# Optimization experiments

Measured on AMD Instinct MI355X. Metric: run time of the kernel, lower is better.

Reference implementation:

```python
import jax, jax.numpy as jnp
import numpy as np

N_LEAVES = 32768
DEPTH = 16               # tree levels, leaves at level 0
N_NODES = 2 * N_LEAVES - 1
H = 256                  # h_size
X = 300                  # x_size
FEAT = 1024              # image feature_size
R = 49                   # image regions
VOCAB = 30000
CLASSES = 5


def setup_inputs() -> dict:
    ks = jax.random.split(jax.random.key(0), 10)
    wordid = jax.random.randint(ks[0], (N_NODES,), 0, VOCAB, dtype=jnp.int32)
    # leaves carry word tokens (mask=1), internal nodes don't (mask=0)
    mask = jnp.concatenate([jnp.ones(N_LEAVES, jnp.int32),
                            jnp.zeros(N_NODES - N_LEAVES, jnp.int32)])
    image = jax.random.normal(ks[1], (R, FEAT), dtype=jnp.float32)
    h0 = jnp.zeros((N_NODES, H), jnp.float32)
    c0 = jnp.zeros((N_NODES, H), jnp.float32)
    s = lambda k, shp, fan: jax.random.normal(k, shp, dtype=jnp.float32) * (1.0 / np.sqrt(fan))
    emb = s(ks[2], (VOCAB, X), X)
    attn_w_in = s(ks[3], (X, FEAT), FEAT)            # Attention.linear_in (no bias)
    attn_w_out = s(ks[4], (X, X + FEAT), X + FEAT)   # Attention.linear_out
    attn_b_out = jnp.zeros((X,), jnp.float32)
    w_iou = s(ks[5], (3 * H, X), X)                  # cell.W_iou (no bias)
    u_iou = s(ks[6], (3 * H, 2 * H), 2 * H)          # cell.U_iou (no bias)
    b_iou = jnp.zeros((1, 3 * H), jnp.float32)
    u_f_w = s(ks[7], (2 * H, 2 * H), 2 * H)          # cell.U_f
    u_f_b = jnp.zeros((2 * H,), jnp.float32)
    lin_w = s(ks[8], (CLASSES, H), H)                # final classifier
    lin_b = jnp.zeros((CLASSES,), jnp.float32)
    return dict(wordid=wordid, mask=mask, image=image, h0=h0, c0=c0, emb=emb,
                attn_w_in=attn_w_in, attn_w_out=attn_w_out, attn_b_out=attn_b_out,
                w_iou=w_iou, u_iou=u_iou, b_iou=b_iou, u_f_w=u_f_w, u_f_b=u_f_b,
                lin_w=lin_w, lin_b=lin_b)


def _forward(wordid, mask, image, h0, c0, emb, attn_w_in, attn_w_out, attn_b_out,
             w_iou, u_iou, b_iou, u_f_w, u_f_b, lin_w, lin_b):
    # --- embedding + attention over image regions ---
    embeds = emb[wordid * mask]                                  # [N, X]
    img_in = image @ attn_w_in.T                                 # [R, X]
    atten = jax.nn.softmax(embeds @ img_in.T, axis=1)            # [N, R]
    context = atten @ image                                      # [N, FEAT]
    sent = jnp.tanh(jnp.concatenate([context, embeds], axis=1) @ attn_w_out.T + attn_b_out)
    iou_x = (sent @ w_iou.T) * mask[:, None].astype(sent.dtype)  # [N, 3H] (dropout p=0 -> identity)

    def apply_node(iou, c_in):
        i, o, u = jnp.split(iou + b_iou, 3, axis=1)
        c_new = jax.nn.sigmoid(i) * jnp.tanh(u) + c_in
        return jax.nn.sigmoid(o) * jnp.tanh(c_new), c_new

    # --- leaves: no mailbox, apply_node with initial c ---
    h_leaf, c_leaf = apply_node(iou_x[:N_LEAVES], c0[:N_LEAVES])
    h = h0.at[:N_LEAVES].set(h_leaf)
    c = c0.at[:N_LEAVES].set(c_leaf)

    # --- topological propagation, one dense level at a time ---
    off_prev, sz, off = 0, N_LEAVES, N_LEAVES
    for _ in range(DEPTH - 1):
        sz_new = sz // 2
        h_cat = jax.lax.dynamic_slice_in_dim(h, off_prev, sz).reshape(sz_new, 2 * H)
        c_ch = jax.lax.dynamic_slice_in_dim(c, off_prev, sz).reshape(sz_new, 2, H)
        f = jax.nn.sigmoid(h_cat @ u_f_w.T + u_f_b).reshape(sz_new, 2, H)
        c_red = jnp.sum(f * c_ch, axis=1)                        # [sz_new, H]
        iou = h_cat @ u_iou.T                                    # reduce_func overwrites node iou
        h_new, c_new = apply_node(iou, c_red)
        h = h.at[off:off + sz_new].set(h_new)
        c = c.at[off:off + sz_new].set(c_new)
        off_prev, sz, off = off, sz_new, off + sz_new

    return h @ lin_w.T + lin_b                                   # [N, CLASSES]


def reference(wordid, mask, image, h0, c0, emb, attn_w_in, attn_w_out, attn_b_out,
              w_iou, u_iou, b_iou, u_f_w, u_f_b, lin_w, lin_b):
    return _forward(wordid, mask, image, h0, c0, emb, attn_w_in, attn_w_out, attn_b_out,
                    w_iou, u_iou, b_iou, u_f_w, u_f_b, lin_w, lin_b)
```

## Files before the change

### kernel.cpp

```cpp
#include <hip/hip_runtime.h>
#include <hip/hip_bf16.h>
#include <math.h>

#define N_LEAVES 32768
#define N_NODES  65535
#define DEPTH    16
#define H        256
#define XS       300
#define FEAT     1024
#define RR       49
#define CLASSES  5

#define XP 320
#define CATW 384

typedef __attribute__((ext_vector_type(8))) short bf16x8;
typedef __attribute__((ext_vector_type(4))) float f32x4;

__device__ __forceinline__ ushort f2bf(float v) {
    __hip_bfloat16 h = __float2bfloat16(v);
    return *reinterpret_cast<ushort*>(&h);
}
__device__ __forceinline__ float bf2f(ushort u) {
    __hip_bfloat16 h; *reinterpret_cast<ushort*>(&h) = u;
    return __bfloat162float(h);
}

__device__ __forceinline__ float fsig(float x) {
    float e = __builtin_amdgcn_exp2f(-1.44269504f * x);
    return __builtin_amdgcn_rcpf(1.0f + e);
}
__device__ __forceinline__ float ftanh(float x) {
    float xx = fmaxf(x, -20.0f);
    float e = __builtin_amdgcn_exp2f(-2.88539008f * xx);
    return (1.0f - e) * __builtin_amdgcn_rcpf(1.0f + e);
}
__device__ __forceinline__ float fexp(float x) {
    return __builtin_amdgcn_exp2f(1.44269504f * x);
}

#define SPIN() __builtin_amdgcn_sched_barrier(0)
#define SBAR() { __builtin_amdgcn_s_barrier(); __builtin_amdgcn_sched_barrier(0); }

__device__ __forceinline__ void swz_mj(int& mblk, int& jg) {
    int lid = blockIdx.y * gridDim.x + blockIdx.x;
    int mcount = gridDim.y, njg = gridDim.x;
    if ((mcount & 7) == 0) {
        int xcd = lid & 7, q = lid >> 3;
        jg = q % njg;
        mblk = xcd * (mcount >> 3) + q / njg;
    } else { mblk = blockIdx.y; jg = blockIdx.x; }
}

__device__ __forceinline__ ushort* lds_at(ushort* base, int row, int kbyte) {
    int off = row * 128 + kbyte;
    off ^= ((row & 7) << 4);
    return (ushort*)((char*)base + off);
}

__device__ __forceinline__ void gll16(const void* g, void* l) {
    __builtin_amdgcn_global_load_lds(
        (const __attribute__((address_space(1))) unsigned int*)g,
        (__attribute__((address_space(3))) unsigned int*)l, 16, 0, 0);
}

__device__ __forceinline__ void issue_tileA(const ushort* A, long lda, long m0, long mmax,
                                            int k0, ushort* buf, int R, int w, int lane)
{
    const int insts = R >> 5;
#pragma unroll
    for (int q = 0; q < 4; ++q) {
        if (q >= insts) break;
        int dest = (w * insts + q) * 1024;
        int row = (dest >> 7) + (lane >> 3);
        int kb = ((lane & 7) << 4) ^ ((row & 7) << 4);
        long am = m0 + row; if (am > mmax) am = mmax;
        gll16((const char*)(A + am * lda + k0) + kb, (char*)buf + dest);
    }
}

__global__ __launch_bounds__(256)
void k_sent(const ushort* __restrict__ A, const ushort* __restrict__ Wf,
            const float* __restrict__ bias, ushort* __restrict__ Cbf)
{
    __shared__ ushort At[3][128 * 64];
    const int tid = threadIdx.x;
    const int l = tid & 63;
    const int w = tid >> 6;
    int mblk, nb; swz_mj(mblk, nb);
    const long m0 = (long)mblk * 128;
    const ushort* wb = Wf + (size_t)(nb * 4 + w) * 24 * 512 + l * 8;

    bf16x8 wreg[2][2][2];
    f32x4 acc[2][8] = {};

    auto loadW = [&](int t, int buf) {
        const ushort* wt = wb + (long)t * 4 * 512;
#pragma unroll
        for (int kk = 0; kk < 2; ++kk)
#pragma unroll
            for (int j = 0; j < 2; ++j)
                wreg[buf][kk][j] = *(const bf16x8*)(wt + (long)(kk * 2 + j) * 512);
    };

    issue_tileA(A, CATW, m0, N_LEAVES - 1, 0, At[0], 128, w, l);
    __syncthreads();
    issue_tileA(A, CATW, m0, N_LEAVES - 1, 64, At[1], 128, w, l);
    SPIN();
    loadW(0, 0);
#pragma unroll
    for (int t = 0; t < 6; ++t) {
        if (t + 2 < 6) issue_tileA(A, CATW, m0, N_LEAVES - 1, (t + 2) * 64, At[(t + 2) % 3], 128, w, l);
        SPIN();
        if (t + 1 < 6) loadW(t + 1, (t + 1) & 1);
        ushort* Ab = At[t % 3];
#pragma unroll
        for (int kk = 0; kk < 2; ++kk) {
            bf16x8 af[8];
#pragma unroll
            for (int i = 0; i < 8; ++i)
                af[i] = *(const bf16x8*)lds_at(Ab, i * 16 + (l & 15), kk * 64 + (l >> 4) * 16);
#pragma unroll
            for (int j = 0; j < 2; ++j)
#pragma unroll
                for (int i = 0; i < 8; ++i)
                    acc[j][i] = __builtin_amdgcn_mfma_f32_16x16x32_bf16(af[i], wreg[t & 1][kk][j], acc[j][i], 0, 0, 0);
        }
        if (t + 1 < 6) SBAR();
    }
#pragma unroll
    for (int j = 0; j < 2; ++j) {
        long n = (long)nb * 128 + w * 32 + j * 16 + (l & 15);
        if (n >= XS) continue;
        float bn = bias[n];
#pragma unroll
        for (int i = 0; i < 8; ++i)
#pragma unroll
            for (int r = 0; r < 4; ++r) {
                long m = m0 + i * 16 + (l >> 4) * 4 + r;
                Cbf[m * XP + n] = f2bf(ftanh(acc[j][i][r] + bn));
            }
    }
}

__global__ __launch_bounds__(256)
void k_attn(const float* __restrict__ emb, const int* __restrict__ wid,
            const ushort* __restrict__ img, ushort* __restrict__ cat)
{
    __shared__ ushort At[128 * 64];
    __shared__ ushort Bt[64 * 64];
    const int tid = threadIdx.x;
    const int l = tid & 63;
    const int w = tid >> 6;
    const long m0 = (long)blockIdx.x * 128;
    const int srow = tid >> 3, skg = tid & 7;

    int wrd[4];
#pragma unroll
    for (int q = 0; q < 4; ++q) wrd[q] = wid[m0 + q * 32 + srow];

    float av[4][8];
    bf16x8 breg[2];
    f32x4 acc[2][4] = {};

    auto loadAB = [&](int t) {
        int c = t * 64 + skg * 8;
#pragma unroll
        for (int q = 0; q < 4; ++q) {
            const float* er = emb + (long)wrd[q] * XS;
            if (c + 8 <= XS) {
                float4 a = *(const float4*)(er + c);
                float4 b = *(const float4*)(er + c + 4);
                av[q][0] = a.x; av[q][1] = a.y; av[q][2] = a.z; av[q][3] = a.w;
                av[q][4] = b.x; av[q][5] = b.y; av[q][6] = b.z; av[q][7] = b.w;
            } else {
#pragma unroll
                for (int u = 0; u < 8; ++u) av[q][u] = (c + u < XS) ? er[c + u] : 0.f;
            }
        }
#pragma unroll
        for (int q = 0; q < 2; ++q)
            breg[q] = *(const bf16x8*)(img + (long)(q * 32 + srow) * XP + t * 64 + skg * 8);
    };
    auto writeAB = [&](int t) {
        int c = t * 64 + skg * 8;
#pragma unroll
        for (int q = 0; q < 4; ++q) {
            int row = q * 32 + srow;
            bf16x8 pk;
#pragma unroll
            for (int u = 0; u < 8; ++u) pk[u] = (short)f2bf(av[q][u]);
            *(bf16x8*)lds_at(At, row, skg * 16) = pk;
            *(bf16x8*)(cat + (m0 + row) * CATW + 64 + c) = pk;
        }
#pragma unroll
        for (int q = 0; q < 2; ++q)
            *(bf16x8*)lds_at(Bt, q * 32 + srow, skg * 16) = breg[q];
    };

    loadAB(0);
    writeAB(0);
    for (int t = 0; t < 5; ++t) {
        __syncthreads();
        if (t + 1 < 5) loadAB(t + 1);
#pragma unroll
        for (int kk = 0; kk < 2; ++kk) {
            bf16x8 af[2], bg[4];
#pragma unroll
            for (int i = 0; i < 2; ++i)
                af[i] = *(const bf16x8*)lds_at(At, w * 32 + i * 16 + (l & 15), kk * 64 + (l >> 4) * 16);
#pragma unroll
            for (int j = 0; j < 4; ++j)
                bg[j] = *(const bf16x8*)lds_at(Bt, j * 16 + (l & 15), kk * 64 + (l >> 4) * 16);
#pragma unroll
            for (int i = 0; i < 2; ++i)
#pragma unroll
                for (int j = 0; j < 4; ++j)
                    acc[i][j] = __builtin_amdgcn_mfma_f32_16x16x32_bf16(af[i], bg[j], acc[i][j], 0, 0, 0);
        }
        if (t + 1 < 5) {
            __syncthreads();
            writeAB(t + 1);
        }
    }
#pragma unroll
    for (int i = 0; i < 2; ++i)
#pragma unroll
        for (int r = 0; r < 4; ++r) {
            long m = m0 + w * 32 + i * 16 + (l >> 4) * 4 + r;
            float v[4]; float mx = -1e30f;
#pragma unroll
            for (int j = 0; j < 4; ++j) {
                int n = j * 16 + (l & 15);
                v[j] = (n < RR) ? acc[i][j][r] : -1e30f;
                mx = fmaxf(mx, v[j]);
            }
#pragma unroll
            for (int sh = 1; sh < 16; sh <<= 1) mx = fmaxf(mx, __shfl_xor(mx, sh));
            float e[4], s = 0.f;
#pragma unroll
            for (int j = 0; j < 4; ++j) { e[j] = fexp(v[j] - mx); s += e[j]; }
#pragma unroll
            for (int sh = 1; sh < 16; sh <<= 1) s += __shfl_xor(s, sh);
            float inv = __builtin_amdgcn_rcpf(s);
#pragma unroll
            for (int j = 0; j < 4; ++j)
                cat[m * CATW + j * 16 + (l & 15)] = f2bf(e[j] * inv);
        }
}

__global__ __launch_bounds__(256)
void k_leaf_fused(const ushort* __restrict__ A, const ushort* __restrict__ Wf,
                  const float* __restrict__ b_iou,
                  ushort* __restrict__ h, ushort* __restrict__ c)
{
    __shared__ ushort At[3][128 * 64];
    const int tid = threadIdx.x;
    const int l = tid & 63;
    const int w = tid >> 6;
    int mblk, jg; swz_mj(mblk, jg);
    const long m0 = (long)mblk * 128;
    const ushort* wb = Wf + (size_t)(jg * 4 + w) * 30 * 512 + l * 8;

    bf16x8 wreg[2][2][3];
    f32x4 acc[3][8] = {};

    auto loadW = [&](int t, int buf) {
        const ushort* wt = wb + (long)t * 6 * 512;
#pragma unroll
        for (int kk = 0; kk < 2; ++kk)
#pragma unroll
            for (int g = 0; g < 3; ++g)
                wreg[buf][kk][g] = *(const bf16x8*)(wt + (long)(kk * 3 + g) * 512);
    };

    issue_tileA(A, XP, m0, N_LEAVES - 1, 0, At[0], 128, w, l);
    __syncthreads();
    issue_tileA(A, XP, m0, N_LEAVES - 1, 64, At[1], 128, w, l);
    SPIN();
    loadW(0, 0);
#pragma unroll
    for (int t = 0; t < 5; ++t) {
        if (t + 2 < 5) issue_tileA(A, XP, m0, N_LEAVES - 1, (t + 2) * 64, At[(t + 2) % 3], 128, w, l);
        SPIN();
        if (t + 1 < 5) loadW(t + 1, (t + 1) & 1);
        ushort* Ab = At[t % 3];
#pragma unroll
        for (int kk = 0; kk < 2; ++kk) {
            bf16x8 af[8];
#pragma unroll
            for (int i = 0; i < 8; ++i)
                af[i] = *(const bf16x8*)lds_at(Ab, i * 16 + (l & 15), kk * 64 + (l >> 4) * 16);
#pragma unroll
            for (int g = 0; g < 3; ++g)
#pragma unroll
                for (int i = 0; i < 8; ++i)
                    acc[g][i] = __builtin_amdgcn_mfma_f32_16x16x32_bf16(af[i], wreg[t & 1][kk][g], acc[g][i], 0, 0, 0);
        }
        if (t + 1 < 5) SBAR();
    }
    {
        int jglob = jg * 64 + w * 16 + (l & 15);
        float bi = b_iou[jglob], bu = b_iou[512 + jglob], bo = b_iou[256 + jglob];
#pragma unroll
        for (int i = 0; i < 8; ++i)
#pragma unroll
            for (int r = 0; r < 4; ++r) {
                long m = m0 + i * 16 + (l >> 4) * 4 + r;
                float cn = fsig(acc[0][i][r] + bi) * ftanh(acc[1][i][r] + bu);
                c[m * H + jglob] = f2bf(cn);
                h[m * H + jglob] = f2bf(fsig(acc[2][i][r] + bo) * ftanh(cn));
            }
    }
}

__global__ __launch_bounds__(256)
void k_tree_fused(const ushort* __restrict__ A, const ushort* __restrict__ Wf,
                  const float* __restrict__ u_f_b, const float* __restrict__ b_iou,
                  const ushort* __restrict__ csrc,
                  ushort* __restrict__ hdst, ushort* __restrict__ cdst, int sz_new)
{
    __shared__ ushort At[3][64 * 64];
    const int tid = threadIdx.x;
    const int l = tid & 63;
    const int w = tid >> 6;
    int mblk, jg; swz_mj(mblk, jg);
    const long m0 = (long)mblk * 64;
    const ushort* wb = Wf + (size_t)(jg * 4 + w) * 80 * 512 + l * 8;

    bf16x8 wreg[2][2][5];
    f32x4 acc[5][4] = {};

    auto loadW = [&](int t, int buf) {
        const ushort* wt = wb + (long)t * 10 * 512;
#pragma unroll
        for (int kk = 0; kk < 2; ++kk)
#pragma unroll
            for (int g = 0; g < 5; ++g)
                wreg[buf][kk][g] = *(const bf16x8*)(wt + (long)(kk * 5 + g) * 512);
    };

    issue_tileA(A, 512, m0, sz_new - 1, 0, At[0], 64, w, l);
    __syncthreads();
    issue_tileA(A, 512, m0, sz_new - 1, 64, At[1], 64, w, l);
    SPIN();
    loadW(0, 0);
#pragma unroll
    for (int t = 0; t < 8; ++t) {
        if (t + 2 < 8) issue_tileA(A, 512, m0, sz_new - 1, (t + 2) * 64, At[(t + 2) % 3], 64, w, l);
        SPIN();
        if (t + 1 < 8) loadW(t + 1, (t + 1) & 1);
        ushort* Ab = At[t % 3];
#pragma unroll
        for (int kk = 0; kk < 2; ++kk) {
            bf16x8 af[4];
#pragma unroll
            for (int i = 0; i < 4; ++i)
                af[i] = *(const bf16x8*)lds_at(Ab, i * 16 + (l & 15), kk * 64 + (l >> 4) * 16);
#pragma unroll
            for (int g = 0; g < 5; ++g)
#pragma unroll
                for (int i = 0; i < 4; ++i)
                    acc[g][i] = __builtin_amdgcn_mfma_f32_16x16x32_bf16(af[i], wreg[t & 1][kk][g], acc[g][i], 0, 0, 0);
        }
        if (t + 1 < 8) SBAR();
    }
    {
        int jglob = jg * 64 + w * 16 + (l & 15);
        float bf0 = u_f_b[jglob], bf1 = u_f_b[256 + jglob];
        float bi = b_iou[jglob], bu = b_iou[512 + jglob], bo = b_iou[256 + jglob];
#pragma unroll
        for (int i = 0; i < 4; ++i)
#pragma unroll
            for (int r = 0; r < 4; ++r) {
                long m = m0 + i * 16 + (l >> 4) * 4 + r;
                if (m < sz_new) {
                    float cl = bf2f(csrc[(2 * m) * H + jglob]);
                    float cr = bf2f(csrc[(2 * m + 1) * H + jglob]);
                    float S = fsig(acc[0][i][r] + bf0) * cl
                            + fsig(acc[1][i][r] + bf1) * cr;
                    float cn = fsig(acc[2][i][r] + bi) * ftanh(acc[3][i][r] + bu) + S;
                    cdst[m * H + jglob] = f2bf(cn);
                    hdst[m * H + jglob] = f2bf(fsig(acc[4][i][r] + bo) * ftanh(cn));
                }
            }
    }
}

__global__ __launch_bounds__(256)
void k_prep(const float* __restrict__ image, const float* __restrict__ w_in,
            const float* __restrict__ w_out, ushort* __restrict__ img_bf,
            ushort* __restrict__ wcat)
{
    const int wave = (blockIdx.x * 256 + threadIdx.x) >> 6;
    const int lane = threadIdx.x & 63;
    const int half = RR * XS;
    if (wave >= 2 * half) return;
    const float* wr; const float* ir; ushort* outp;
    if (wave < half) {
        int r = wave / XS, x = wave % XS;
        ir = image + (long)r * FEAT;
        wr = w_in + (long)x * FEAT;
        outp = img_bf + (long)r * XP + x;
    } else {
        int w2 = wave - half;
        int x = w2 / RR, r = w2 % RR;
        ir = image + (long)r * FEAT;
        wr = w_out + (long)x * (FEAT + XS);
        outp = wcat + (long)x * CATW + r;
    }
    float s = 0.f;
#pragma unroll
    for (int u = 0; u < FEAT / 64; ++u) {
        int f = lane + u * 64;
        s = fmaf(ir[f], wr[f], s);
    }
#pragma unroll
    for (int sh = 32; sh; sh >>= 1) s += __shfl_xor(s, sh);
    if (lane == 0) *outp = f2bf(s);
}

__global__ __launch_bounds__(256)
void k_cvt(ushort* __restrict__ dst, long dld, long doff,
           const float* __restrict__ src, long sld, long soff,
           int rows, int cols)
{
    long idx = (long)blockIdx.x * 256 + threadIdx.x;
    if (idx >= (long)rows * cols) return;
    int r = (int)(idx / cols), c = (int)(idx % cols);
    dst[r * dld + doff + c] = f2bf(src[r * sld + soff + c]);
}

__global__ __launch_bounds__(256)
void k_bld_wcatf(ushort* __restrict__ dst, const ushort* __restrict__ wcat)
{
    long idx = (long)blockIdx.x * 256 + threadIdx.x;
    if (idx >= 147456) return;
    int u = idx & 7; long r = idx >> 3;
    int l = r & 63; r >>= 6;
    int j = r & 1; r >>= 1;
    int kk = r & 1; r >>= 1;
    int t = (int)(r % 6); r /= 6;
    int wq = r & 3; r >>= 2;
    int nb = (int)r;
    int row = nb * 128 + wq * 32 + j * 16 + (l & 15);
    int col = t * 64 + kk * 32 + (l >> 4) * 8 + u;
    dst[idx] = wcat[(long)row * CATW + col];
}

__global__ __launch_bounds__(256)
void k_bld_w3f(ushort* __restrict__ dst, const float* __restrict__ w_iou)
{
    long idx = (long)blockIdx.x * 256 + threadIdx.x;
    if (idx >= 245760) return;
    int u = idx & 7; long r = idx >> 3;
    int l = r & 63; r >>= 6;
    int g = (int)(r % 3); r /= 3;
    int kk = r & 1; r >>= 1;
    int t = (int)(r % 5); r /= 5;
    int wq = r & 3; r >>= 2;
    int jg = (int)r;
    int row = jg * 64 + wq * 16 + (l & 15);
    int col = t * 64 + kk * 32 + (l >> 4) * 8 + u;
    int srow = (g == 0) ? row : (g == 1) ? 512 + row : 256 + row;
    dst[idx] = (col < XS) ? f2bf(w_iou[(long)srow * XS + col]) : 0;
}

__global__ __launch_bounds__(256)
void k_bld_w5f(ushort* __restrict__ dst, const float* __restrict__ u_f_w,
               const float* __restrict__ u_iou)
{
    long idx = (long)blockIdx.x * 256 + threadIdx.x;
    if (idx >= 655360) return;
    int u = idx & 7; long r = idx >> 3;
    int l = r & 63; r >>= 6;
    int g = (int)(r % 5); r /= 5;
    int kk = r & 1; r >>= 1;
    int t = (int)(r & 7); r >>= 3;
    int wq = r & 3; r >>= 2;
    int jg = (int)r;
    int row = jg * 64 + wq * 16 + (l & 15);
    int col = t * 64 + kk * 32 + (l >> 4) * 8 + u;
    const float* src;
    if (g == 0)      src = u_f_w + (long)row * 512;
    else if (g == 1) src = u_f_w + (long)(256 + row) * 512;
    else if (g == 2) src = u_iou + (long)row * 512;
    else if (g == 3) src = u_iou + (long)(512 + row) * 512;
    else             src = u_iou + (long)(256 + row) * 512;
    dst[idx] = f2bf(src[col]);
}

__global__ __launch_bounds__(256)
void k_classify(const ushort* __restrict__ h, const float* __restrict__ lin_w,
                const float* __restrict__ lin_b, float* __restrict__ out, int n_rows)
{
    const int node = (int)((blockIdx.x * 256 + threadIdx.x) >> 6);
    const int lane = threadIdx.x & 63;
    if (node >= n_rows) return;
    const ushort* hr = h + (long)node * H;
    float p[CLASSES] = {0.f};
#pragma unroll
    for (int u = 0; u < H / 64; ++u) {
        int j = lane + u * 64;
        float hv = bf2f(hr[j]);
#pragma unroll
        for (int cc = 0; cc < CLASSES; ++cc)
            p[cc] = fmaf(hv, lin_w[cc * H + j], p[cc]);
    }
#pragma unroll
    for (int cc = 0; cc < CLASSES; ++cc)
#pragma unroll
        for (int sh = 32; sh; sh >>= 1) p[cc] += __shfl_xor(p[cc], sh);
    if (lane == 0) {
#pragma unroll
        for (int cc = 0; cc < CLASSES; ++cc)
            out[(long)node * CLASSES + cc] = p[cc] + lin_b[cc];
    }
}

extern "C" void kernel_launch(void* const* d_in, const int* in_sizes, int n_in,
                              void* d_out, int out_size, void* d_ws, size_t ws_size,
                              hipStream_t stream)
{
    const int*   wordid     = (const int*)  d_in[0];
    const float* image      = (const float*)d_in[2];
    const float* emb        = (const float*)d_in[5];
    const float* attn_w_in  = (const float*)d_in[6];
    const float* attn_w_out = (const float*)d_in[7];
    const float* attn_b_out = (const float*)d_in[8];
    const float* w_iou      = (const float*)d_in[9];
    const float* u_iou      = (const float*)d_in[10];
    const float* b_iou      = (const float*)d_in[11];
    const float* u_f_w      = (const float*)d_in[12];
    const float* u_f_b      = (const float*)d_in[13];
    const float* lin_w      = (const float*)d_in[14];
    const float* lin_b      = (const float*)d_in[15];
    float* out = (float*)d_out;

    char* p = (char*)d_ws;
    auto alloc = [&](size_t bytes) { char* r = p; p += (bytes + 255) & ~255UL; return r; };
    ushort* cat     = (ushort*)alloc((size_t)N_LEAVES * CATW * 2);
    ushort* sentbf  = (ushort*)alloc((size_t)N_LEAVES * XP * 2);
    ushort* hall    = (ushort*)alloc((size_t)65536 * H * 2);
    ushort* cA      = (ushort*)alloc((size_t)N_LEAVES * H * 2);
    ushort* cB      = (ushort*)alloc((size_t)(N_LEAVES/2) * H * 2);
    ushort* img_bf  = (ushort*)alloc((size_t)64 * XP * 2);
    ushort* wcat    = (ushort*)alloc((size_t)CATW * CATW * 2);
    ushort* wcatf   = (ushort*)alloc((size_t)147456 * 2);
    ushort* w3f     = (ushort*)alloc((size_t)245760 * 2);
    ushort* w5f     = (ushort*)alloc((size_t)655360 * 2);
    (void)ws_size;

    hipMemsetAsync(img_bf, 0, (size_t)64 * XP * 2, stream);
    hipMemsetAsync(wcat,   0, (size_t)CATW * CATW * 2, stream);
    {
        int waves = 2 * RR * XS;
        k_prep<<<(waves * 64 + 255) / 256, 256, 0, stream>>>(image, attn_w_in,
                                                             attn_w_out, img_bf, wcat);
    }
    k_cvt<<<((long)XS * XS + 255) / 256, 256, 0, stream>>>(
        wcat, CATW, 64, attn_w_out, FEAT + XS, FEAT, XS, XS);
    k_bld_wcatf<<<(147456 + 255) / 256, 256, 0, stream>>>(wcatf, wcat);
    k_bld_w3f<<<(245760 + 255) / 256, 256, 0, stream>>>(w3f, w_iou);
    k_bld_w5f<<<(655360 + 255) / 256, 256, 0, stream>>>(w5f, u_f_w, u_iou);

    k_attn<<<N_LEAVES / 128, 256, 0, stream>>>(emb, wordid, img_bf, cat);
    k_sent<<<dim3(3, N_LEAVES / 128), 256, 0, stream>>>(cat, wcatf, attn_b_out, sentbf);
    k_leaf_fused<<<dim3(4, N_LEAVES / 128), 256, 0, stream>>>(
        sentbf, w3f, b_iou, hall, cA);

    ushort* csrc = cA; ushort* cdst = cB;
    int node_off = N_LEAVES;
    int sz = N_LEAVES;
    int off_prev = 0;
    for (int lvl = 0; lvl < DEPTH - 1; ++lvl) {
        int sz_new = sz / 2;
        k_tree_fused<<<dim3(4, (sz_new + 63) / 64), 256, 0, stream>>>(
            hall + (long)off_prev * H, w5f, u_f_b, b_iou, csrc,
            hall + (long)node_off * H, cdst, sz_new);
        off_prev = node_off;
        node_off += sz_new;
        ushort* t = csrc; csrc = cdst; cdst = t;
        sz = sz_new;
    }

    k_classify<<<((long)N_NODES * 64 + 255) / 256, 256, 0, stream>>>(
        hall, lin_w, lin_b, out, N_NODES);
}
```

Baseline: 315.4 us.

## Fuse attention, sentence projection and leaf cell into one LDS-resident kernel

Replaces the three leaf-stage kernels (attention softmax, sentence linear_out+tanh, leaf iou cell) with one kernel. Each block keeps 64 leaves' embeddings, attention weights and sentence vectors in shared memory, which removes the global round-trips through the cat and sentbf buffers. Image features are pre-swizzled into MFMA fragment order so they load directly into registers. It also vectorises the classifier loads. The cost is a smaller M tile with weights streamed per block, plus fewer blocks with more serial work each, which may lower MFMA efficiency and occupancy.

```diff
diff --git a/kernel.cpp b/kernel.cpp
--- a/kernel.cpp
+++ b/kernel.cpp
@@ -80,236 +80,189 @@
 }
 
 __global__ __launch_bounds__(256)
-void k_sent(const ushort* __restrict__ A, const ushort* __restrict__ Wf,
-            const float* __restrict__ bias, ushort* __restrict__ Cbf)
-{
-    __shared__ ushort At[3][128 * 64];
+void k_asl(const float* __restrict__ emb, const int* __restrict__ wid,
+           const ushort* __restrict__ imgf, const ushort* __restrict__ wcatf,
+           const float* __restrict__ bias, const ushort* __restrict__ w3f,
+           const float* __restrict__ b_iou,
+           ushort* __restrict__ h, ushort* __restrict__ c)
+{
+    __shared__ ushort E[5][64 * 64];
+    __shared__ ushort Atn[64 * 64];
     const int tid = threadIdx.x;
     const int l = tid & 63;
     const int w = tid >> 6;
-    int mblk, nb; swz_mj(mblk, nb);
-    const long m0 = (long)mblk * 128;
-    const ushort* wb = Wf + (size_t)(nb * 4 + w) * 24 * 512 + l * 8;
-
-    bf16x8 wreg[2][2][2];
-    f32x4 acc[2][8] = {};
-
-    auto loadW = [&](int t, int buf) {
-        const ushort* wt = wb + (long)t * 4 * 512;
+    const long m0 = (long)blockIdx.x * 64;
+
+    {
+        int row = tid >> 2;
+        int q = tid & 3;
+        const float* er = emb + (long)wid[m0 + row] * XS;
+#pragma unroll
+        for (int u = 0; u < 10; ++u) {
+            int ccol = q * 80 + u * 8;
+            bf16x8 pk;
+            if (ccol + 8 <= XS) {
+                float4 a = *(const float4*)(er + ccol);
+                float4 b = *(const float4*)(er + ccol + 4);
+                pk[0] = (short)f2bf(a.x); pk[1] = (short)f2bf(a.y);
+                pk[2] = (short)f2bf(a.z); pk[3] = (short)f2bf(a.w);
+                pk[4] = (short)f2bf(b.x); pk[5] = (short)f2bf(b.y);
+                pk[6] = (short)f2bf(b.z); pk[7] = (short)f2bf(b.w);
+            } else {
+#pragma unroll
+                for (int e = 0; e < 8; ++e)
+                    pk[e] = (ccol + e < XS) ? (short)f2bf(er[ccol + e]) : (short)0;
+            }
+            *(bf16x8*)lds_at(E[ccol >> 6], row, (ccol & 63) * 2) = pk;
+        }
+    }
+    __syncthreads();
+
+    {
+        f32x4 sacc[4] = {};
+        const ushort* ib = imgf + l * 8;
+#pragma unroll
+        for (int t = 0; t < 5; ++t)
+#pragma unroll
+            for (int kk = 0; kk < 2; ++kk) {
+                bf16x8 af = *(const bf16x8*)lds_at(E[t], w * 16 + (l & 15), kk * 64 + (l >> 4) * 16);
+#pragma unroll
+                for (int j = 0; j < 4; ++j) {
+                    bf16x8 bg = *(const bf16x8*)(ib + (long)((j * 5 + t) * 2 + kk) * 512);
+                    sacc[j] = __builtin_amdgcn_mfma_f32_16x16x32_bf16(af, bg, sacc[j], 0, 0, 0);
+                }
+            }
+#pragma unroll
+        for (int r = 0; r < 4; ++r) {
+            int row = w * 16 + (l >> 4) * 4 + r;
+            float v[4]; float mx = -1e30f;
+#pragma unroll
+            for (int j = 0; j < 4; ++j) {
+                int n = j * 16 + (l & 15);
+                v[j] = (n < RR) ? sacc[j][r] : -1e30f;
+                mx = fmaxf(mx, v[j]);
+            }
+#pragma unroll
+            for (int sh = 1; sh < 16; sh <<= 1) mx = fmaxf(mx, __shfl_xor(mx, sh));
+            float e[4], s = 0.f;
+#pragma unroll
+            for (int j = 0; j < 4; ++j) { e[j] = fexp(v[j] - mx); s += e[j]; }
+#pragma unroll
+            for (int sh = 1; sh < 16; sh <<= 1) s += __shfl_xor(s, sh);
+            float inv = __builtin_amdgcn_rcpf(s);
+#pragma unroll
+            for (int j = 0; j < 4; ++j)
+                *lds_at(Atn, row, (j * 16 + (l & 15)) * 2) = f2bf(e[j] * inv);
+        }
+    }
+    __syncthreads();
+
+    f32x4 acc3[3][2][4] = {};
+#pragma unroll
+    for (int ng = 0; ng < 3; ++ng) {
+        const ushort* wbn = wcatf + (size_t)(ng * 4 + w) * 24 * 512 + l * 8;
+        bf16x8 wcur[2][2], wnxt[2][2];
 #pragma unroll
         for (int kk = 0; kk < 2; ++kk)
 #pragma unroll
             for (int j = 0; j < 2; ++j)
-                wreg[buf][kk][j] = *(const bf16x8*)(wt + (long)(kk * 2 + j) * 512);
-    };
-
-    issue_tileA(A, CATW, m0, N_LEAVES - 1, 0, At[0], 128, w, l);
+                wcur[kk][j] = *(const bf16x8*)(wbn + (long)(kk * 2 + j) * 512);
+#pragma unroll
+        for (int t = 0; t < 6; ++t) {
+            if (t + 1 < 6)
+#pragma unroll
+                for (int kk = 0; kk < 2; ++kk)
+#pragma unroll
+                    for (int j = 0; j < 2; ++j)
+                        wnxt[kk][j] = *(const bf16x8*)(wbn + (long)((t + 1) * 4 + kk * 2 + j) * 512);
+            ushort* Ab = (t == 0) ? Atn : E[t - 1];
+#pragma unroll
+            for (int kk = 0; kk < 2; ++kk) {
+                bf16x8 af[4];
+#pragma unroll
+                for (int i = 0; i < 4; ++i)
+                    af[i] = *(const bf16x8*)lds_at(Ab, i * 16 + (l & 15), kk * 64 + (l >> 4) * 16);
+#pragma unroll
+                for (int j = 0; j < 2; ++j)
+#pragma unroll
+                    for (int i = 0; i < 4; ++i)
+                        acc3[ng][j][i] = __builtin_amdgcn_mfma_f32_16x16x32_bf16(
+                            af[i], wcur[kk][j], acc3[ng][j][i], 0, 0, 0);
+            }
+#pragma unroll
+            for (int kk = 0; kk < 2; ++kk)
+#pragma unroll
+                for (int j = 0; j < 2; ++j)
+                    wcur[kk][j] = wnxt[kk][j];
+        }
+    }
     __syncthreads();
-    issue_tileA(A, CATW, m0, N_LEAVES - 1, 64, At[1], 128, w, l);
-    SPIN();
-    loadW(0, 0);
-#pragma unroll
-    for (int t = 0; t < 6; ++t) {
-        if (t + 2 < 6) issue_tileA(A, CATW, m0, N_LEAVES - 1, (t + 2) * 64, At[(t + 2) % 3], 128, w, l);
-        SPIN();
-        if (t + 1 < 6) loadW(t + 1, (t + 1) & 1);
-        ushort* Ab = At[t % 3];
-#pragma unroll
-        for (int kk = 0; kk < 2; ++kk) {
-            bf16x8 af[8];
-#pragma unroll
-            for (int i = 0; i < 8; ++i)
-                af[i] = *(const bf16x8*)lds_at(Ab, i * 16 + (l & 15), kk * 64 + (l >> 4) * 16);
-#pragma unroll
-            for (int j = 0; j < 2; ++j)
-#pragma unroll
-                for (int i = 0; i < 8; ++i)
-                    acc[j][i] = __builtin_amdgcn_mfma_f32_16x16x32_bf16(af[i], wreg[t & 1][kk][j], acc[j][i], 0, 0, 0);
+
+#pragma unroll
+    for (int ng = 0; ng < 3; ++ng)
+#pragma unroll
+        for (int j = 0; j < 2; ++j) {
+            int n = ng * 128 + w * 32 + j * 16 + (l & 15);
+            if (n >= XP) continue;
+            float bn = (n < XS) ? bias[n] : 0.f;
+#pragma unroll
+            for (int i = 0; i < 4; ++i)
+#pragma unroll
+                for (int r = 0; r < 4; ++r) {
+                    int row = i * 16 + (l >> 4) * 4 + r;
+                    float v = (n < XS) ? ftanh(acc3[ng][j][i][r] + bn) : 0.f;
+                    *lds_at(E[n >> 6], row, (n & 63) * 2) = f2bf(v);
+                }
         }
-        if (t + 1 < 6) SBAR();
-    }
-#pragma unroll
-    for (int j = 0; j < 2; ++j) {
-        long n = (long)nb * 128 + w * 32 + j * 16 + (l & 15);
-        if (n >= XS) continue;
-        float bn = bias[n];
-#pragma unroll
-        for (int i = 0; i < 8; ++i)
+    __syncthreads();
+
+#pragma unroll
+    for (int jf = 0; jf < 4; ++jf) {
+        const ushort* wbj = w3f + (size_t)(w * 4 + jf) * 30 * 512 + l * 8;
+        f32x4 lacc[3][4] = {};
+        bf16x8 wcur[2][3], wnxt[2][3];
+#pragma unroll
+        for (int kk = 0; kk < 2; ++kk)
+#pragma unroll
+            for (int g = 0; g < 3; ++g)
+                wcur[kk][g] = *(const bf16x8*)(wbj + (long)(kk * 3 + g) * 512);
+#pragma unroll
+        for (int t = 0; t < 5; ++t) {
+            if (t + 1 < 5)
+#pragma unroll
+                for (int kk = 0; kk < 2; ++kk)
+#pragma unroll
+                    for (int g = 0; g < 3; ++g)
+                        wnxt[kk][g] = *(const bf16x8*)(wbj + (long)((t + 1) * 6 + kk * 3 + g) * 512);
+#pragma unroll
+            for (int kk = 0; kk < 2; ++kk) {
+                bf16x8 af[4];
+#pragma unroll
+                for (int i = 0; i < 4; ++i)
+                    af[i] = *(const bf16x8*)lds_at(E[t], i * 16 + (l & 15), kk * 64 + (l >> 4) * 16);
+#pragma unroll
+                for (int g = 0; g < 3; ++g)
+#pragma unroll
+                    for (int i = 0; i < 4; ++i)
+                        lacc[g][i] = __builtin_amdgcn_mfma_f32_16x16x32_bf16(
+                            af[i], wcur[kk][g], lacc[g][i], 0, 0, 0);
+            }
+#pragma unroll
+            for (int kk = 0; kk < 2; ++kk)
+#pragma unroll
+                for (int g = 0; g < 3; ++g)
+                    wcur[kk][g] = wnxt[kk][g];
+        }
+        int jglob = w * 64 + jf * 16 + (l & 15);
+        float bi = b_iou[jglob], bu = b_iou[512 + jglob], bo = b_iou[256 + jglob];
+#pragma unroll
+        for (int i = 0; i < 4; ++i)
 #pragma unroll
             for (int r = 0; r < 4; ++r) {
                 long m = m0 + i * 16 + (l >> 4) * 4 + r;
-                Cbf[m * XP + n] = f2bf(ftanh(acc[j][i][r] + bn));
-            }
-    }
-}
-
-__global__ __launch_bounds__(256)
-void k_attn(const float* __restrict__ emb, const int* __restrict__ wid,
-            const ushort* __restrict__ img, ushort* __restrict__ cat)
-{
-    __shared__ ushort At[128 * 64];
-    __shared__ ushort Bt[64 * 64];
-    const int tid = threadIdx.x;
-    const int l = tid & 63;
-    const int w = tid >> 6;
-    const long m0 = (long)blockIdx.x * 128;
-    const int srow = tid >> 3, skg = tid & 7;
-
-    int wrd[4];
-#pragma unroll
-    for (int q = 0; q < 4; ++q) wrd[q] = wid[m0 + q * 32 + srow];
-
-    float av[4][8];
-    bf16x8 breg[2];
-    f32x4 acc[2][4] = {};
-
-    auto loadAB = [&](int t) {
-        int c = t * 64 + skg * 8;
-#pragma unroll
-        for (int q = 0; q < 4; ++q) {
-            const float* er = emb + (long)wrd[q] * XS;
-            if (c + 8 <= XS) {
-                float4 a = *(const float4*)(er + c);
-                float4 b = *(const float4*)(er + c + 4);
-                av[q][0] = a.x; av[q][1] = a.y; av[q][2] = a.z; av[q][3] = a.w;
-                av[q][4] = b.x; av[q][5] = b.y; av[q][6] = b.z; av[q][7] = b.w;
-            } else {
-#pragma unroll
-                for (int u = 0; u < 8; ++u) av[q][u] = (c + u < XS) ? er[c + u] : 0.f;
-            }
-        }
-#pragma unroll
-        for (int q = 0; q < 2; ++q)
-            breg[q] = *(const bf16x8*)(img + (long)(q * 32 + srow) * XP + t * 64 + skg * 8);
-    };
-    auto writeAB = [&](int t) {
-        int c = t * 64 + skg * 8;
-#pragma unroll
-        for (int q = 0; q < 4; ++q) {
-            int row = q * 32 + srow;
-            bf16x8 pk;
-#pragma unroll
-            for (int u = 0; u < 8; ++u) pk[u] = (short)f2bf(av[q][u]);
-            *(bf16x8*)lds_at(At, row, skg * 16) = pk;
-            *(bf16x8*)(cat + (m0 + row) * CATW + 64 + c) = pk;
-        }
-#pragma unroll
-        for (int q = 0; q < 2; ++q)
-            *(bf16x8*)lds_at(Bt, q * 32 + srow, skg * 16) = breg[q];
-    };
-
-    loadAB(0);
-    writeAB(0);
-    for (int t = 0; t < 5; ++t) {
-        __syncthreads();
-        if (t + 1 < 5) loadAB(t + 1);
-#pragma unroll
-        for (int kk = 0; kk < 2; ++kk) {
-            bf16x8 af[2], bg[4];
-#pragma unroll
-            for (int i = 0; i < 2; ++i)
-                af[i] = *(const bf16x8*)lds_at(At, w * 32 + i * 16 + (l & 15), kk * 64 + (l >> 4) * 16);
-#pragma unroll
-            for (int j = 0; j < 4; ++j)
-                bg[j] = *(const bf16x8*)lds_at(Bt, j * 16 + (l & 15), kk * 64 + (l >> 4) * 16);
-#pragma unroll
-            for (int i = 0; i < 2; ++i)
-#pragma unroll
-                for (int j = 0; j < 4; ++j)
-                    acc[i][j] = __builtin_amdgcn_mfma_f32_16x16x32_bf16(af[i], bg[j], acc[i][j], 0, 0, 0);
-        }
-        if (t + 1 < 5) {
-            __syncthreads();
-            writeAB(t + 1);
-        }
-    }
-#pragma unroll
-    for (int i = 0; i < 2; ++i)
-#pragma unroll
-        for (int r = 0; r < 4; ++r) {
-            long m = m0 + w * 32 + i * 16 + (l >> 4) * 4 + r;
-            float v[4]; float mx = -1e30f;
-#pragma unroll
-            for (int j = 0; j < 4; ++j) {
-                int n = j * 16 + (l & 15);
-                v[j] = (n < RR) ? acc[i][j][r] : -1e30f;
-                mx = fmaxf(mx, v[j]);
-            }
-#pragma unroll
-            for (int sh = 1; sh < 16; sh <<= 1) mx = fmaxf(mx, __shfl_xor(mx, sh));
-            float e[4], s = 0.f;
-#pragma unroll
-            for (int j = 0; j < 4; ++j) { e[j] = fexp(v[j] - mx); s += e[j]; }
-#pragma unroll
-            for (int sh = 1; sh < 16; sh <<= 1) s += __shfl_xor(s, sh);
-            float inv = __builtin_amdgcn_rcpf(s);
-#pragma unroll
-            for (int j = 0; j < 4; ++j)
-                cat[m * CATW + j * 16 + (l & 15)] = f2bf(e[j] * inv);
-        }
-}
-
-__global__ __launch_bounds__(256)
-void k_leaf_fused(const ushort* __restrict__ A, const ushort* __restrict__ Wf,
-                  const float* __restrict__ b_iou,
-                  ushort* __restrict__ h, ushort* __restrict__ c)
-{
-    __shared__ ushort At[3][128 * 64];
-    const int tid = threadIdx.x;
-    const int l = tid & 63;
-    const int w = tid >> 6;
-    int mblk, jg; swz_mj(mblk, jg);
-    const long m0 = (long)mblk * 128;
-    const ushort* wb = Wf + (size_t)(jg * 4 + w) * 30 * 512 + l * 8;
-
-    bf16x8 wreg[2][2][3];
-    f32x4 acc[3][8] = {};
-
-    auto loadW = [&](int t, int buf) {
-        const ushort* wt = wb + (long)t * 6 * 512;
-#pragma unroll
-        for (int kk = 0; kk < 2; ++kk)
-#pragma unroll
-            for (int g = 0; g < 3; ++g)
-                wreg[buf][kk][g] = *(const bf16x8*)(wt + (long)(kk * 3 + g) * 512);
-    };
-
-    issue_tileA(A, XP, m0, N_LEAVES - 1, 0, At[0], 128, w, l);
-    __syncthreads();
-    issue_tileA(A, XP, m0, N_LEAVES - 1, 64, At[1], 128, w, l);
-    SPIN();
-    loadW(0, 0);
-#pragma unroll
-    for (int t = 0; t < 5; ++t) {
-        if (t + 2 < 5) issue_tileA(A, XP, m0, N_LEAVES - 1, (t + 2) * 64, At[(t + 2) % 3], 128, w, l);
-        SPIN();
-        if (t + 1 < 5) loadW(t + 1, (t + 1) & 1);
-        ushort* Ab = At[t % 3];
-#pragma unroll
-        for (int kk = 0; kk < 2; ++kk) {
-            bf16x8 af[8];
-#pragma unroll
-            for (int i = 0; i < 8; ++i)
-                af[i] = *(const bf16x8*)lds_at(Ab, i * 16 + (l & 15), kk * 64 + (l >> 4) * 16);
-#pragma unroll
-            for (int g = 0; g < 3; ++g)
-#pragma unroll
-                for (int i = 0; i < 8; ++i)
-                    acc[g][i] = __builtin_amdgcn_mfma_f32_16x16x32_bf16(af[i], wreg[t & 1][kk][g], acc[g][i], 0, 0, 0);
-        }
-        if (t + 1 < 5) SBAR();
-    }
-    {
-        int jglob = jg * 64 + w * 16 + (l & 15);
-        float bi = b_iou[jglob], bu = b_iou[512 + jglob], bo = b_iou[256 + jglob];
-#pragma unroll
-        for (int i = 0; i < 8; ++i)
-#pragma unroll
-            for (int r = 0; r < 4; ++r) {
-                long m = m0 + i * 16 + (l >> 4) * 4 + r;
-                float cn = fsig(acc[0][i][r] + bi) * ftanh(acc[1][i][r] + bu);
+                float cn = fsig(lacc[0][i][r] + bi) * ftanh(lacc[1][i][r] + bu);
                 c[m * H + jglob] = f2bf(cn);
-                h[m * H + jglob] = f2bf(fsig(acc[2][i][r] + bo) * ftanh(cn));
+                h[m * H + jglob] = f2bf(fsig(lacc[2][i][r] + bo) * ftanh(cn));
             }
     }
 }
@@ -429,6 +382,21 @@
     if (idx >= (long)rows * cols) return;
     int r = (int)(idx / cols), c = (int)(idx % cols);
     dst[r * dld + doff + c] = f2bf(src[r * sld + soff + c]);
+}
+
+__global__ __launch_bounds__(256)
+void k_bld_imgf(ushort* __restrict__ dst, const ushort* __restrict__ img_bf)
+{
+    long idx = (long)blockIdx.x * 256 + threadIdx.x;
+    if (idx >= 20480) return;
+    int u = idx & 7; long r = idx >> 3;
+    int l = r & 63; r >>= 6;
+    int kk = r & 1; r >>= 1;
+    int t = (int)(r % 5); r /= 5;
+    int j = (int)r;
+    int row = j * 16 + (l & 15);
+    int col = t * 64 + kk * 32 + (l >> 4) * 8 + u;
+    dst[idx] = img_bf[(long)row * XP + col];
 }
 
 __global__ __launch_bounds__(256)
@@ -497,15 +465,13 @@
     const int node = (int)((blockIdx.x * 256 + threadIdx.x) >> 6);
     const int lane = threadIdx.x & 63;
     if (node >= n_rows) return;
-    const ushort* hr = h + (long)node * H;
-    float p[CLASSES] = {0.f};
-#pragma unroll
-    for (int u = 0; u < H / 64; ++u) {
-        int j = lane + u * 64;
-        float hv = bf2f(hr[j]);
-#pragma unroll
-        for (int cc = 0; cc < CLASSES; ++cc)
-            p[cc] = fmaf(hv, lin_w[cc * H + j], p[cc]);
+    ushort4 hv4 = *(const ushort4*)(h + (long)node * H + lane * 4);
+    float hv[4] = { bf2f(hv4.x), bf2f(hv4.y), bf2f(hv4.z), bf2f(hv4.w) };
+    float p[CLASSES];
+#pragma unroll
+    for (int cc = 0; cc < CLASSES; ++cc) {
+        float4 wv = *(const float4*)(lin_w + (long)cc * H + lane * 4);
+        p[cc] = hv[0] * wv.x + hv[1] * wv.y + hv[2] * wv.z + hv[3] * wv.w;
     }
 #pragma unroll
     for (int cc = 0; cc < CLASSES; ++cc)
@@ -539,13 +505,12 @@
 
     char* p = (char*)d_ws;
     auto alloc = [&](size_t bytes) { char* r = p; p += (bytes + 255) & ~255UL; return r; };
-    ushort* cat     = (ushort*)alloc((size_t)N_LEAVES * CATW * 2);
-    ushort* sentbf  = (ushort*)alloc((size_t)N_LEAVES * XP * 2);
     ushort* hall    = (ushort*)alloc((size_t)65536 * H * 2);
     ushort* cA      = (ushort*)alloc((size_t)N_LEAVES * H * 2);
     ushort* cB      = (ushort*)alloc((size_t)(N_LEAVES/2) * H * 2);
     ushort* img_bf  = (ushort*)alloc((size_t)64 * XP * 2);
     ushort* wcat    = (ushort*)alloc((size_t)CATW * CATW * 2);
+    ushort* imgf    = (ushort*)alloc((size_t)20480 * 2);
     ushort* wcatf   = (ushort*)alloc((size_t)147456 * 2);
     ushort* w3f     = (ushort*)alloc((size_t)245760 * 2);
     ushort* w5f     = (ushort*)alloc((size_t)655360 * 2);
@@ -560,14 +525,13 @@
     }
     k_cvt<<<((long)XS * XS + 255) / 256, 256, 0, stream>>>(
         wcat, CATW, 64, attn_w_out, FEAT + XS, FEAT, XS, XS);
+    k_bld_imgf<<<(20480 + 255) / 256, 256, 0, stream>>>(imgf, img_bf);
     k_bld_wcatf<<<(147456 + 255) / 256, 256, 0, stream>>>(wcatf, wcat);
     k_bld_w3f<<<(245760 + 255) / 256, 256, 0, stream>>>(w3f, w_iou);
     k_bld_w5f<<<(655360 + 255) / 256, 256, 0, stream>>>(w5f, u_f_w, u_iou);
 
-    k_attn<<<N_LEAVES / 128, 256, 0, stream>>>(emb, wordid, img_bf, cat);
-    k_sent<<<dim3(3, N_LEAVES / 128), 256, 0, stream>>>(cat, wcatf, attn_b_out, sentbf);
-    k_leaf_fused<<<dim3(4, N_LEAVES / 128), 256, 0, stream>>>(
-        sentbf, w3f, b_iou, hall, cA);
+    k_asl<<<N_LEAVES / 64, 256, 0, stream>>>(emb, wordid, imgf, wcatf,
+                                             attn_b_out, w3f, b_iou, hall, cA);
 
     ushort* csrc = cA; ushort* cdst = cB;
     int node_off = N_LEAVES;
```

New measurement: 333.2 us. 1.06x slower.
